# Performance work log

Hardware: AMD Instinct MI355X
Metric: run time of the kernel (lower is better)

## Reference

```python
import jax, jax.numpy as jnp
import numpy as np

DIM = 512
BATCH = 1024
# row-major upper-triangle (i<j) index pairs, matching the original nested loop order
_IU, _JU = np.triu_indices(DIM, k=1)
_IU = jnp.asarray(_IU)
_JU = jnp.asarray(_JU)
FEAT_DIM = DIM + DIM * (DIM - 1) // 2 + DIM  # 131840


def setup_inputs() -> dict:
    key = jax.random.key(0)
    k1, k2, k3 = jax.random.split(key, 3)
    x = jax.random.normal(k1, (BATCH, DIM), dtype=jnp.float32)
    W = jax.random.normal(k2, (1, FEAT_DIM), dtype=jnp.float32) / np.sqrt(FEAT_DIM).astype(np.float32)
    b = jax.random.normal(k3, (1,), dtype=jnp.float32)
    return {"x": x, "W": W, "b": b}


def _quadratic_features(x):
    # pairwise products x_i * x_j for i<j in the original loop order, then squares
    pairs = x[:, _IU] * x[:, _JU]          # [B, dim*(dim-1)/2]
    squares = x * x                        # [B, dim]
    return jnp.concatenate([pairs, squares], axis=1)


def reference(x, W, b):
    feats = jnp.concatenate([x, _quadratic_features(x)], axis=1)  # [B, FEAT_DIM]
    logits = feats @ W.T + b                                      # [B, 1]
    return jax.nn.sigmoid(logits)
```

## Files before the change

kernel.cpp:

```cpp
#include <hip/hip_runtime.h>
#include <math.h>

#define DIM 512
#define BATCH 1024
#define NPAIR (DIM * (DIM - 1) / 2)

typedef short bf16x8 __attribute__((ext_vector_type(8)));
typedef float f32x4  __attribute__((ext_vector_type(4)));

__device__ __forceinline__ unsigned short f2bf(float f) {
    unsigned int u = __float_as_uint(f);
    u += 0x7fff + ((u >> 16) & 1);
    return (unsigned short)(u >> 16);
}
__device__ __forceinline__ float bf2f(unsigned short h) {
    return __uint_as_float(((unsigned int)h) << 16);
}


__global__ __launch_bounds__(256)
void quad_gemm(const float* __restrict__ x, const float* __restrict__ W,
               float* __restrict__ partial) {
    const int bid   = blockIdx.x;
    const int m_blk = bid / 20;
    const int p     = bid - m_blk * 20;
    const int n_blk = (p < 2) ? 0 : (p < 6) ? 1 : (p < 12) ? 2 : 3;
    const int kb    = (p < 2) ? 0 : (p < 6) ? 2 : (p < 12) ? 6 : 12;
    const int kspl  = p - kb;
    const int row0 = m_blk * 64, n0 = n_blk * 128, k0 = kspl * 64;

    const int tid = threadIdx.x;
    const int lane = tid & 63, w = tid >> 6;
    const int wm = w >> 1, wn = w & 1;
    const int r15 = lane & 15, q = lane >> 4;

    const float* Wp  = W + DIM;
    const float* Wsq = W + DIM + NPAIR;

    __shared__ alignas(16) unsigned short sAh[64 * 64];
    __shared__ alignas(16) unsigned short sAl[64 * 64];
    __shared__ alignas(16) unsigned short sBh[128 * 64];
    __shared__ alignas(16) unsigned short sBl[128 * 64];

    {
        const int row = tid >> 2;
        const float* src = x + (size_t)(row0 + row) * DIM + k0;
        #pragma unroll
        for (int u = 0; u < 2; ++u) {
            const int c = (tid & 3) + u * 4;
            const float4 v0 = *(const float4*)(src + c * 8);
            const float4 v1 = *(const float4*)(src + c * 8 + 4);
            const float vs[8] = {v0.x, v0.y, v0.z, v0.w, v1.x, v1.y, v1.z, v1.w};
            bf16x8 hv, lv;
            #pragma unroll
            for (int e = 0; e < 8; ++e) {
                unsigned short h = f2bf(vs[e]);
                hv[e] = (short)h;
                lv[e] = (short)f2bf(vs[e] - bf2f(h));
            }
            const int loff = row * 64 + ((c ^ (row & 7)) * 8);
            *(bf16x8*)(sAh + loff) = hv;
            *(bf16x8*)(sAl + loff) = lv;
        }
    }

    {
        const int nr = tid & 127;
        const int n  = n0 + nr;
        const int cb = (tid >> 7) * 4;
        #pragma unroll
        for (int u = 0; u < 4; ++u) {
            const int c = cb + u;
            float vs[8];
            int k  = k0 + c * 8;
            int ro = k * (DIM - 2) - (k * (k - 1)) / 2 - 1;
            #pragma unroll
            for (int e = 0; e < 8; ++e) {
                const float wv = Wp[ro + n];
                vs[e] = (n > k) ? wv : ((n == k) ? Wsq[k] : 0.f);
                ro += DIM - 2 - k;
                ++k;
            }
            bf16x8 hv, lv;
            #pragma unroll
            for (int e = 0; e < 8; ++e) {
                unsigned short h = f2bf(vs[e]);
                hv[e] = (short)h;
                lv[e] = (short)f2bf(vs[e] - bf2f(h));
            }
            const int loff = nr * 64 + ((c ^ (nr & 7)) * 8);
            *(bf16x8*)(sBh + loff) = hv;
            *(bf16x8*)(sBl + loff) = lv;
        }
    }
    __syncthreads();

    f32x4 acc[2][4];
    #pragma unroll
    for (int i = 0; i < 2; ++i)
        #pragma unroll
        for (int j = 0; j < 4; ++j) acc[i][j] = (f32x4){0.f, 0.f, 0.f, 0.f};

    #pragma unroll
    for (int ks = 0; ks < 2; ++ks) {
        const int c = ks * 4 + q;
        bf16x8 ah[2], al[2];
        #pragma unroll
        for (int sm = 0; sm < 2; ++sm) {
            const int row = wm * 32 + sm * 16 + r15;
            const int off = row * 64 + ((c ^ (row & 7)) * 8);
            ah[sm] = *(const bf16x8*)(sAh + off);
            al[sm] = *(const bf16x8*)(sAl + off);
        }
        #pragma unroll
        for (int sn = 0; sn < 4; ++sn) {
            const int row = wn * 64 + sn * 16 + r15;
            const int off = row * 64 + ((c ^ (row & 7)) * 8);
            const bf16x8 bh = *(const bf16x8*)(sBh + off);
            const bf16x8 bl = *(const bf16x8*)(sBl + off);
            acc[0][sn] = __builtin_amdgcn_mfma_f32_16x16x32_bf16(ah[0], bh, acc[0][sn], 0, 0, 0);
            acc[1][sn] = __builtin_amdgcn_mfma_f32_16x16x32_bf16(ah[1], bh, acc[1][sn], 0, 0, 0);
            acc[0][sn] = __builtin_amdgcn_mfma_f32_16x16x32_bf16(al[0], bh, acc[0][sn], 0, 0, 0);
            acc[1][sn] = __builtin_amdgcn_mfma_f32_16x16x32_bf16(al[1], bh, acc[1][sn], 0, 0, 0);
            acc[0][sn] = __builtin_amdgcn_mfma_f32_16x16x32_bf16(ah[0], bl, acc[0][sn], 0, 0, 0);
            acc[1][sn] = __builtin_amdgcn_mfma_f32_16x16x32_bf16(ah[1], bl, acc[1][sn], 0, 0, 0);
        }
    }

    float yl[2][4];
    #pragma unroll
    for (int i = 0; i < 2; ++i)
        #pragma unroll
        for (int r = 0; r < 4; ++r) yl[i][r] = 0.f;

    #pragma unroll
    for (int sn = 0; sn < 4; ++sn) {
        const int n = n0 + wn * 64 + sn * 16 + r15;
        const float wlv = (kspl == 0) ? W[n] : 0.f;
        #pragma unroll
        for (int sm = 0; sm < 2; ++sm) {
            const int mbase = row0 + wm * 32 + sm * 16 + q * 4;
            #pragma unroll
            for (int r = 0; r < 4; ++r) {
                const float xv = x[(size_t)(mbase + r) * DIM + n];
                yl[sm][r] += (acc[sm][sn][r] + wlv) * xv;
            }
        }
    }
    #pragma unroll
    for (int off = 1; off < 16; off <<= 1) {
        #pragma unroll
        for (int sm = 0; sm < 2; ++sm)
            #pragma unroll
            for (int r = 0; r < 4; ++r)
                yl[sm][r] += __shfl_xor(yl[sm][r], off);
    }
    const int slot = p * 2 + wn;
    if (r15 == 0) {
        #pragma unroll
        for (int sm = 0; sm < 2; ++sm)
            #pragma unroll
            for (int r = 0; r < 4; ++r)
                partial[(size_t)slot * BATCH + row0 + wm * 32 + sm * 16 + q * 4 + r] = yl[sm][r];
    }
}

__global__ __launch_bounds__(256)
void finalize(const float* __restrict__ partial, const float* __restrict__ bias,
              float* __restrict__ out) {
    const int t = blockIdx.x * 256 + threadIdx.x;
    float z = bias[0];
    #pragma unroll 8
    for (int s = 0; s < 40; ++s) z += partial[(size_t)s * BATCH + t];
    out[t] = 1.0f / (1.0f + expf(-z));
}

extern "C" void kernel_launch(void* const* d_in, const int* in_sizes, int n_in,
                              void* d_out, int out_size, void* d_ws, size_t ws_size,
                              hipStream_t stream) {
    const float* x = (const float*)d_in[0];
    const float* W = (const float*)d_in[1];
    const float* b = (const float*)d_in[2];
    float* out = (float*)d_out;

    float* partial = (float*)d_ws;

    hipLaunchKernelGGL(quad_gemm, dim3(320), dim3(256), 0, stream, x, W, partial);
    hipLaunchKernelGGL(finalize,  dim3(BATCH / 256), dim3(256), 0, stream, partial, b, out);
}
```

Measured before the change: 15.11 us.

## Double block size to eight waves and reduce partials in shared memory

```diff
diff --git a/kernel.cpp b/kernel.cpp
--- a/kernel.cpp
+++ b/kernel.cpp
@@ -4,6 +4,7 @@
 #define DIM 512
 #define BATCH 1024
 #define NPAIR (DIM * (DIM - 1) / 2)
+#define TPB 512
 
 typedef short bf16x8 __attribute__((ext_vector_type(8)));
 typedef float f32x4  __attribute__((ext_vector_type(4)));
@@ -18,7 +19,7 @@
 }
 
 
-__global__ __launch_bounds__(256)
+__global__ __launch_bounds__(TPB)
 void quad_gemm(const float* __restrict__ x, const float* __restrict__ W,
                float* __restrict__ partial) {
     const int bid   = blockIdx.x;
@@ -31,7 +32,7 @@
 
     const int tid = threadIdx.x;
     const int lane = tid & 63, w = tid >> 6;
-    const int wm = w >> 1, wn = w & 1;
+    const int wm = w >> 2, wn = w & 3;
     const int r15 = lane & 15, q = lane >> 4;
 
     const float* Wp  = W + DIM;
@@ -41,35 +42,33 @@
     __shared__ alignas(16) unsigned short sAl[64 * 64];
     __shared__ alignas(16) unsigned short sBh[128 * 64];
     __shared__ alignas(16) unsigned short sBl[128 * 64];
+    __shared__ float ysum[4][64];
 
     {
-        const int row = tid >> 2;
-        const float* src = x + (size_t)(row0 + row) * DIM + k0;
-        #pragma unroll
-        for (int u = 0; u < 2; ++u) {
-            const int c = (tid & 3) + u * 4;
-            const float4 v0 = *(const float4*)(src + c * 8);
-            const float4 v1 = *(const float4*)(src + c * 8 + 4);
-            const float vs[8] = {v0.x, v0.y, v0.z, v0.w, v1.x, v1.y, v1.z, v1.w};
-            bf16x8 hv, lv;
-            #pragma unroll
-            for (int e = 0; e < 8; ++e) {
-                unsigned short h = f2bf(vs[e]);
-                hv[e] = (short)h;
-                lv[e] = (short)f2bf(vs[e] - bf2f(h));
-            }
-            const int loff = row * 64 + ((c ^ (row & 7)) * 8);
-            *(bf16x8*)(sAh + loff) = hv;
-            *(bf16x8*)(sAl + loff) = lv;
-        }
+        const int row = tid >> 3;
+        const int c   = tid & 7;
+        const float* src = x + (size_t)(row0 + row) * DIM + k0 + c * 8;
+        const float4 v0 = *(const float4*)(src);
+        const float4 v1 = *(const float4*)(src + 4);
+        const float vs[8] = {v0.x, v0.y, v0.z, v0.w, v1.x, v1.y, v1.z, v1.w};
+        bf16x8 hv, lv;
+        #pragma unroll
+        for (int e = 0; e < 8; ++e) {
+            unsigned short h = f2bf(vs[e]);
+            hv[e] = (short)h;
+            lv[e] = (short)f2bf(vs[e] - bf2f(h));
+        }
+        const int loff = row * 64 + ((c ^ (row & 7)) * 8);
+        *(bf16x8*)(sAh + loff) = hv;
+        *(bf16x8*)(sAl + loff) = lv;
     }
 
     {
         const int nr = tid & 127;
         const int n  = n0 + nr;
-        const int cb = (tid >> 7) * 4;
-        #pragma unroll
-        for (int u = 0; u < 4; ++u) {
+        const int cb = (tid >> 7) * 2;
+        #pragma unroll
+        for (int u = 0; u < 2; ++u) {
             const int c = cb + u;
             float vs[8];
             int k  = k0 + c * 8;
@@ -93,13 +92,28 @@
             *(bf16x8*)(sBl + loff) = lv;
         }
     }
+
+    float xv[2][2][4];
+    float wlv[2];
+    #pragma unroll
+    for (int sn = 0; sn < 2; ++sn) {
+        const int n = n0 + wn * 32 + sn * 16 + r15;
+        wlv[sn] = (kspl == 0) ? W[n] : 0.f;
+        #pragma unroll
+        for (int sm = 0; sm < 2; ++sm) {
+            const int mbase = row0 + wm * 32 + sm * 16 + q * 4;
+            #pragma unroll
+            for (int r = 0; r < 4; ++r)
+                xv[sn][sm][r] = x[(size_t)(mbase + r) * DIM + n];
+        }
+    }
     __syncthreads();
 
-    f32x4 acc[2][4];
+    f32x4 acc[2][2];
     #pragma unroll
     for (int i = 0; i < 2; ++i)
         #pragma unroll
-        for (int j = 0; j < 4; ++j) acc[i][j] = (f32x4){0.f, 0.f, 0.f, 0.f};
+        for (int j = 0; j < 2; ++j) acc[i][j] = (f32x4){0.f, 0.f, 0.f, 0.f};
 
     #pragma unroll
     for (int ks = 0; ks < 2; ++ks) {
@@ -113,8 +127,8 @@
             al[sm] = *(const bf16x8*)(sAl + off);
         }
         #pragma unroll
-        for (int sn = 0; sn < 4; ++sn) {
-            const int row = wn * 64 + sn * 16 + r15;
+        for (int sn = 0; sn < 2; ++sn) {
+            const int row = wn * 32 + sn * 16 + r15;
             const int off = row * 64 + ((c ^ (row & 7)) * 8);
             const bf16x8 bh = *(const bf16x8*)(sBh + off);
             const bf16x8 bl = *(const bf16x8*)(sBl + off);
@@ -129,24 +143,18 @@
 
     float yl[2][4];
     #pragma unroll
-    for (int i = 0; i < 2; ++i)
-        #pragma unroll
-        for (int r = 0; r < 4; ++r) yl[i][r] = 0.f;
-
-    #pragma unroll
-    for (int sn = 0; sn < 4; ++sn) {
-        const int n = n0 + wn * 64 + sn * 16 + r15;
-        const float wlv = (kspl == 0) ? W[n] : 0.f;
-        #pragma unroll
-        for (int sm = 0; sm < 2; ++sm) {
-            const int mbase = row0 + wm * 32 + sm * 16 + q * 4;
-            #pragma unroll
-            for (int r = 0; r < 4; ++r) {
-                const float xv = x[(size_t)(mbase + r) * DIM + n];
-                yl[sm][r] += (acc[sm][sn][r] + wlv) * xv;
-            }
-        }
-    }
+    for (int sm = 0; sm < 2; ++sm)
+        #pragma unroll
+        for (int r = 0; r < 4; ++r) yl[sm][r] = 0.f;
+
+    #pragma unroll
+    for (int sn = 0; sn < 2; ++sn)
+        #pragma unroll
+        for (int sm = 0; sm < 2; ++sm)
+            #pragma unroll
+            for (int r = 0; r < 4; ++r)
+                yl[sm][r] += (acc[sm][sn][r] + wlv[sn]) * xv[sn][sm][r];
+
     #pragma unroll
     for (int off = 1; off < 16; off <<= 1) {
         #pragma unroll
@@ -155,13 +163,17 @@
             for (int r = 0; r < 4; ++r)
                 yl[sm][r] += __shfl_xor(yl[sm][r], off);
     }
-    const int slot = p * 2 + wn;
     if (r15 == 0) {
         #pragma unroll
         for (int sm = 0; sm < 2; ++sm)
             #pragma unroll
             for (int r = 0; r < 4; ++r)
-                partial[(size_t)slot * BATCH + row0 + wm * 32 + sm * 16 + q * 4 + r] = yl[sm][r];
+                ysum[wn][wm * 32 + sm * 16 + q * 4 + r] = yl[sm][r];
+    }
+    __syncthreads();
+    if (tid < 64) {
+        const float z = (ysum[0][tid] + ysum[1][tid]) + (ysum[2][tid] + ysum[3][tid]);
+        partial[(size_t)p * BATCH + row0 + tid] = z;
     }
 }
 
@@ -170,8 +182,8 @@
               float* __restrict__ out) {
     const int t = blockIdx.x * 256 + threadIdx.x;
     float z = bias[0];
-    #pragma unroll 8
-    for (int s = 0; s < 40; ++s) z += partial[(size_t)s * BATCH + t];
+    #pragma unroll
+    for (int s = 0; s < 20; ++s) z += partial[(size_t)s * BATCH + t];
     out[t] = 1.0f / (1.0f + expf(-z));
 }
 
@@ -185,6 +197,6 @@
 
     float* partial = (float*)d_ws;
 
-    hipLaunchKernelGGL(quad_gemm, dim3(320), dim3(256), 0, stream, x, W, partial);
+    hipLaunchKernelGGL(quad_gemm, dim3(320), dim3(TPB), 0, stream, x, W, partial);
     hipLaunchKernelGGL(finalize,  dim3(BATCH / 256), dim3(256), 0, stream, partial, b, out);
 }
```

Result: faster. 13.33 us (-11.7%).
